# Kernel optimization log

Hardware: AMD Instinct MI355X
Metric: run time of the kernel (lower is better)

## Reference

```python
import jax, jax.numpy as jnp
import numpy as np
import math

NUM_HEADS = 16


def _alibi_slopes(n):
    # n is a power of 2 here (16)
    start = 2.0 ** (-2.0 ** (-(math.log2(n) - 3)))
    return jnp.asarray([start * (start ** i) for i in range(n)], dtype=jnp.float32)


def setup_inputs() -> dict:
    key = jax.random.key(0)
    ks = jax.random.split(key, 7)
    B, S, D = 2, 2048, 1024
    s = 0.02
    return {
        "query": jax.random.normal(ks[0], (B, S, D), jnp.float32),
        "key": jax.random.normal(ks[1], (B, S, D), jnp.float32),
        "value": jax.random.normal(ks[2], (B, S, D), jnp.float32),
        "Wq": jax.random.normal(ks[3], (D, D), jnp.float32) * s,
        "Wk": jax.random.normal(ks[4], (D, D), jnp.float32) * s,
        "Wv": jax.random.normal(ks[5], (D, D), jnp.float32) * s,
        "Wo": jax.random.normal(ks[6], (D, D), jnp.float32) * s,
    }


def reference(query, key, value, Wq, Wk, Wv, Wo):
    B, S, D = query.shape
    H = NUM_HEADS
    hd = D // H
    scale = math.sqrt(hd)

    # projections (bias-free linears), split into heads: [B, S, H, hd]
    Q = (query @ Wq).reshape(B, S, H, hd)
    K = (key @ Wk).reshape(B, -1, H, hd)
    V = (value @ Wv).reshape(B, -1, H, hd)

    # attention scores [B, H, S, S]
    scores = jnp.einsum("bqhd,bkhd->bhqk", Q, K) / scale

    # ALiBi bias: -slope_h * |i - j|, broadcast over batch
    pos = jnp.arange(S, dtype=jnp.float32)
    rel = jnp.abs(pos[None, :] - pos[:, None])  # [S, S]
    slopes = _alibi_slopes(H)
    scores = scores - slopes[None, :, None, None] * rel[None, None, :, :]

    attn = jax.nn.softmax(scores, axis=-1)
    out = jnp.einsum("bhqk,bkhd->bqhd", attn, V).reshape(B, S, D)
    return out @ Wo
```

## Files before the change

kernel.cpp:

```cpp
#include <hip/hip_runtime.h>
#include <cstdint>
#include <cstddef>


typedef unsigned short u16;
typedef __attribute__((ext_vector_type(8))) _Float16 half8;
typedef __attribute__((ext_vector_type(8))) unsigned short u16x8;
typedef __attribute__((ext_vector_type(4))) float f32x4;

#define DEVI static __device__ __forceinline__
#define MFMA16(a, b, c) __builtin_amdgcn_mfma_f32_16x16x32_f16(a, b, c, 0, 0, 0)

DEVI u16 f2h_bits(float f) {
  _Float16 h = (_Float16)f;
  union { _Float16 h; u16 u; } v; v.h = h;
  return v.u;
}

DEVI void gl_lds16(const u16* g, u16* l) {
  __builtin_amdgcn_global_load_lds(
      (const __attribute__((address_space(1))) void*)g,
      (__attribute__((address_space(3))) void*)l, 16, 0, 0);
}

__global__ __launch_bounds__(256) void cast3_h(const float* __restrict__ in0,
                                               const float* __restrict__ in1,
                                               const float* __restrict__ in2,
                                               u16* __restrict__ o0,
                                               u16* __restrict__ o1,
                                               u16* __restrict__ o2, int n) {
  const float* in = blockIdx.z == 0 ? in0 : (blockIdx.z == 1 ? in1 : in2);
  u16* out = blockIdx.z == 0 ? o0 : (blockIdx.z == 1 ? o1 : o2);
  int i = (blockIdx.x * 256 + threadIdx.x) * 4;
  if (i + 3 < n) {
    const float4 v = *(const float4*)(in + i);
    ushort4 o;
    o.x = f2h_bits(v.x); o.y = f2h_bits(v.y); o.z = f2h_bits(v.z); o.w = f2h_bits(v.w);
    *(ushort4*)(out + i) = o;
  }
}

__global__ __launch_bounds__(256) void transpose4_h(
    const float* __restrict__ W0, const float* __restrict__ W1,
    const float* __restrict__ W2, const float* __restrict__ W3,
    u16* __restrict__ T0, u16* __restrict__ T1, u16* __restrict__ T2,
    u16* __restrict__ T3) {
  const float* W = blockIdx.z == 0 ? W0 : (blockIdx.z == 1 ? W1 : (blockIdx.z == 2 ? W2 : W3));
  u16* Wt = blockIdx.z == 0 ? T0 : (blockIdx.z == 1 ? T1 : (blockIdx.z == 2 ? T2 : T3));
  __shared__ float tile[32][33];
  const int bx = blockIdx.x * 32;
  const int by = blockIdx.y * 32;
  const int x = threadIdx.x & 31;
  const int y0 = threadIdx.x >> 5;
#pragma unroll
  for (int i = y0; i < 32; i += 8)
    tile[i][x] = W[(size_t)(by + i) * 1024 + bx + x];
  __syncthreads();
#pragma unroll
  for (int i = y0; i < 32; i += 8)
    Wt[(size_t)(bx + i) * 1024 + by + x] = f2h_bits(tile[x][i]);
}

__global__ __launch_bounds__(256) void vtrans(const u16* __restrict__ Vp,
                                              u16* __restrict__ Vt) {
  __shared__ u16 tile[64][72];
  const int t = threadIdx.x;
  const int s0 = blockIdx.x * 64;
  const int bh = blockIdx.y;
  const int b = bh >> 4, h = bh & 15;
#pragma unroll
  for (int it = 0; it < 2; ++it) {
    const int ci = it * 256 + t;
    const int srow = ci >> 3, cc = (ci & 7) << 3;
    const u16x8 v = *(const u16x8*)(Vp + (size_t)(b * 2048 + s0 + srow) * 1024 + h * 64 + cc);
    *(u16x8*)(&tile[srow][cc]) = v;
  }
  __syncthreads();
#pragma unroll
  for (int it = 0; it < 2; ++it) {
    const int ci = it * 256 + t;
    const int drow = ci >> 3, cc = (ci & 7) << 3;
    u16x8 o;
#pragma unroll
    for (int j = 0; j < 8; ++j) o[j] = tile[cc + j][drow];
    *(u16x8*)(Vt + ((size_t)bh * 64 + drow) * 2048 + s0 + cc) = o;
  }
}

DEVI void gemm_body(const u16* __restrict__ A, const u16* __restrict__ Bt,
                    void* __restrict__ Cout, int mode, int kLo, int kHi,
                    u16* As, u16* Bs) {
  constexpr int K = 1024, N = 1024;
  const int t = threadIdx.x;
  const int lane = t & 63;
  const int quad = lane >> 4;
  const int l16 = lane & 15;
  const int wid = t >> 6;
  const int mBase = blockIdx.y * 128;
  const int nBase = blockIdx.x * 128;
  const int wM = (wid >> 1) * 64;
  const int wN = (wid & 1) * 64;
  const int cswz = l16 & 7;

  f32x4 acc[4][4];
#pragma unroll
  for (int i = 0; i < 4; ++i)
#pragma unroll
    for (int j = 0; j < 4; ++j) acc[i][j] = (f32x4){0.f, 0.f, 0.f, 0.f};

  for (int kt = kLo; kt < kHi; ++kt) {
    const int kB = kt * 64;
    __syncthreads();
#pragma unroll
    for (int i = 0; i < 4; ++i) {
      const int ci = i * 256 + t;
      const int row = ci >> 3;
      const int col = (((ci & 7) ^ (row & 7)) << 3);
      gl_lds16(A + (size_t)(mBase + row) * K + kB + col, As + ci * 8);
      gl_lds16(Bt + (size_t)(nBase + row) * K + kB + col, Bs + ci * 8);
    }
    __syncthreads();

#pragma unroll
    for (int kk = 0; kk < 2; ++kk) {
      const int ck = (((kk * 4 + quad) ^ cswz) << 3);
      half8 a[4], b[4];
#pragma unroll
      for (int mi = 0; mi < 4; ++mi)
        a[mi] = *(const half8*)(As + (wM + mi * 16 + l16) * 64 + ck);
#pragma unroll
      for (int ni = 0; ni < 4; ++ni)
        b[ni] = *(const half8*)(Bs + (wN + ni * 16 + l16) * 64 + ck);
#pragma unroll
      for (int mi = 0; mi < 4; ++mi)
#pragma unroll
        for (int ni = 0; ni < 4; ++ni)
          acc[mi][ni] = MFMA16(a[mi], b[ni], acc[mi][ni]);
    }
  }

#pragma unroll
  for (int mi = 0; mi < 4; ++mi) {
#pragma unroll
    for (int ni = 0; ni < 4; ++ni) {
#pragma unroll
      for (int r = 0; r < 4; ++r) {
        const int m = mBase + wM + mi * 16 + quad * 4 + r;
        const int n = nBase + wN + ni * 16 + l16;
        const float v = acc[mi][ni][r];
        if (mode == 0) {
          ((float*)Cout)[(size_t)m * N + n] = v;
        } else {
          ((u16*)Cout)[(size_t)m * N + n] = f2h_bits(v);
        }
      }
    }
  }
}

__global__ __launch_bounds__(256) void proj_qkv(
    const u16* __restrict__ qb, const u16* __restrict__ kb, const u16* __restrict__ vb,
    const u16* __restrict__ Wqt, const u16* __restrict__ Wkt, const u16* __restrict__ Wvt,
    u16* __restrict__ Qp, u16* __restrict__ Kp, u16* __restrict__ Vp) {
  __shared__ u16 As[128 * 64];
  __shared__ u16 Bs[128 * 64];
  const int z = blockIdx.z;
  const u16* A = z == 0 ? qb : (z == 1 ? kb : vb);
  const u16* Bt = z == 0 ? Wqt : (z == 1 ? Wkt : Wvt);
  void* C = z == 0 ? (void*)Qp : (z == 1 ? (void*)Kp : (void*)Vp);
  gemm_body(A, Bt, C, 1, 0, 16, As, Bs);
}

__global__ __launch_bounds__(256) void gemm_out(const u16* __restrict__ Ao,
                                                const u16* __restrict__ Wot,
                                                float* __restrict__ p0,
                                                float* __restrict__ p1) {
  __shared__ u16 As[128 * 64];
  __shared__ u16 Bs[128 * 64];
  const int z = blockIdx.z;
  gemm_body(Ao, Wot, z ? (void*)p1 : (void*)p0, 0, z * 8, z * 8 + 8, As, Bs);
}

__global__ __launch_bounds__(256) void add2(const float* __restrict__ a,
                                            const float* __restrict__ b,
                                            float* __restrict__ o, int n) {
  int i = (blockIdx.x * 256 + threadIdx.x) * 4;
  if (i + 3 < n) {
    float4 x = *(const float4*)(a + i);
    const float4 y = *(const float4*)(b + i);
    x.x += y.x; x.y += y.y; x.z += y.z; x.w += y.w;
    *(float4*)(o + i) = x;
  }
}

__global__ __launch_bounds__(128, 2) void flash_alibi(
    const u16* __restrict__ Qg, const u16* __restrict__ Kg,
    const u16* __restrict__ Vtg, u16* __restrict__ Opart,
    float* __restrict__ lpart) {
  constexpr int S = 2048, Dm = 1024, HD = 64;
  __shared__ u16 Qs[64 * 64];
  __shared__ u16 Ks[2][64 * 64];
  __shared__ u16 Vs[2][64 * 64];
  __shared__ u16 Ps[64 * 64];
  const int t = threadIdx.x, lane = t & 63, wid = t >> 6;
  const int quad = lane >> 4, l16 = lane & 15;
  const int idx = blockIdx.x;
  const int s = 29 - (idx >> 6);
  const int bq = idx & 63;
  const int b = bq >> 5, qt = bq & 31;
  int h, seg, nseg;
  if      (s >= 26) { h = 15; seg = s - 26; nseg = 4; }
  else if (s >= 22) { h = 14; seg = s - 22; nseg = 4; }
  else if (s >= 18) { h = 13; seg = s - 18; nseg = 4; }
  else if (s >= 15) { h = 12; seg = s - 15; nseg = 3; }
  else if (s >= 13) { h = 11; seg = s - 13; nseg = 2; }
  else if (s >= 11) { h = 10; seg = s - 11; nseg = 2; }
  else if (s >= 9)  { h = 9;  seg = s - 9;  nseg = 2; }
  else              { h = s;  seg = 0;      nseg = 1; }
  const int qBase = qt * 64;
  const size_t qRow0 = (size_t)b * S + qBase;
  const float sl2 = __builtin_amdgcn_exp2f(-0.5f * (float)(h + 1)) * 1.44269504f;
  const float sc2 = 0.125f * 1.44269504f;
  const int Di = (int)(22.0f / sl2);
  const int ktLo = max(0, (qBase - Di) >> 6);
  const int ktHi = min(31, (qBase + 63 + Di) >> 6);
  const int W = ktHi - ktLo + 1;
  const int myLo = ktLo + (W * seg) / nseg;
  const int myHi = ktLo + (W * (seg + 1)) / nseg - 1;
  const size_t slotG = (size_t)bq * 30 + s;
  const int cswz = ((l16 & 7) << 3);
  const u16* Kgb = Kg + (size_t)b * S * Dm + h * HD;
  const u16* Vgb = Vtg + (size_t)(b * 16 + h) * HD * S;

#pragma unroll
  for (int i = 0; i < 4; ++i) {
    const int ci = i * 128 + t;
    const int row = ci >> 3, col = (((ci & 7) ^ (row & 7)) << 3);
    gl_lds16(Qg + (qRow0 + row) * Dm + h * HD + col, Qs + ci * 8);
  }
  if (myLo <= myHi) {
#pragma unroll
    for (int i = 0; i < 4; ++i) {
      const int ci = i * 128 + t;
      const int row = ci >> 3, col = (((ci & 7) ^ (row & 7)) << 3);
      gl_lds16(Kgb + (size_t)(myLo * 64 + row) * Dm + col, Ks[0] + ci * 8);
      gl_lds16(Vgb + (size_t)row * S + myLo * 64 + col, Vs[0] + ci * 8);
    }
  }

  float bi[2][4];
#pragma unroll
  for (int m = 0; m < 2; ++m)
#pragma unroll
    for (int r = 0; r < 4; ++r)
      bi[m][r] = sl2 * (float)(qBase + wid * 32 + m * 16 + quad * 4 + r);

  f32x4 acc_o[2][4];
#pragma unroll
  for (int m = 0; m < 2; ++m)
#pragma unroll
    for (int nd = 0; nd < 4; ++nd) acc_o[m][nd] = (f32x4){0.f, 0.f, 0.f, 0.f};
  float lrow[2][4] = {{0.f, 0.f, 0.f, 0.f}, {0.f, 0.f, 0.f, 0.f}};

  const int pRowBase = wid * 32;
  int cur = 0;

  for (int kt = myLo; kt <= myHi; ++kt, cur ^= 1) {
    __asm__ volatile("s_waitcnt vmcnt(0) lgkmcnt(0)\n\ts_barrier" ::: "memory");

    if (kt < myHi) {
      const int kB2 = (kt + 1) * 64;
      u16* Kd = Ks[cur ^ 1];
      u16* Vd = Vs[cur ^ 1];
#pragma unroll
      for (int i = 0; i < 4; ++i) {
        const int ci = i * 128 + t;
        const int row = ci >> 3, col = (((ci & 7) ^ (row & 7)) << 3);
        gl_lds16(Kgb + (size_t)(kB2 + row) * Dm + col, Kd + ci * 8);
        gl_lds16(Vgb + (size_t)row * S + kB2 + col, Vd + ci * 8);
      }
    }

    const int kB = kt * 64;
    f32x4 sc[2][4];
#pragma unroll
    for (int m = 0; m < 2; ++m)
#pragma unroll
      for (int ni = 0; ni < 4; ++ni) sc[m][ni] = (f32x4){0.f, 0.f, 0.f, 0.f};
#pragma unroll
    for (int ks = 0; ks < 2; ++ks) {
      const int ck = ((ks * 4 + quad) << 3) ^ cswz;
      const half8 a0 = *(const half8*)(Qs + (wid * 32 + l16) * HD + ck);
      const half8 a1 = *(const half8*)(Qs + (wid * 32 + 16 + l16) * HD + ck);
#pragma unroll
      for (int ni = 0; ni < 4; ++ni) {
        const half8 bk = *(const half8*)(Ks[cur] + (ni * 16 + l16) * HD + ck);
        sc[0][ni] = MFMA16(a0, bk, sc[0][ni]);
        sc[1][ni] = MFMA16(a1, bk, sc[1][ni]);
      }
    }

    float bj[4];
#pragma unroll
    for (int ni = 0; ni < 4; ++ni) bj[ni] = sl2 * (float)(kB + ni * 16 + l16);
#pragma unroll
    for (int m = 0; m < 2; ++m) {
#pragma unroll
      for (int r = 0; r < 4; ++r) {
        float rs = 0.f;
        const int prow = (pRowBase + m * 16 + quad * 4 + r) * 64;
#pragma unroll
        for (int ni = 0; ni < 4; ++ni) {
          const float d = fabsf(bi[m][r] - bj[ni]);
          const float p = __builtin_amdgcn_exp2f(sc[m][ni][r] * sc2 - d);
          rs += p;
          Ps[prow + ((ni * 16 + l16) ^ (quad << 4))] = f2h_bits(p);
        }
        lrow[m][r] += rs;
      }
    }
    __asm__ volatile("s_waitcnt lgkmcnt(0)" ::: "memory");

#pragma unroll
    for (int ks = 0; ks < 2; ++ks) {
      const int pk = (ks * 32 + quad * 8) ^ ((l16 & 12) << 2);
      const int ck = ((ks * 4 + quad) << 3) ^ cswz;
      const half8 aP0 = *(const half8*)(Ps + (pRowBase + l16) * 64 + pk);
      const half8 aP1 = *(const half8*)(Ps + (pRowBase + 16 + l16) * 64 + pk);
#pragma unroll
      for (int nd = 0; nd < 4; ++nd) {
        const half8 bv = *(const half8*)(Vs[cur] + (nd * 16 + l16) * HD + ck);
        acc_o[0][nd] = MFMA16(aP0, bv, acc_o[0][nd]);
        acc_o[1][nd] = MFMA16(aP1, bv, acc_o[1][nd]);
      }
    }
  }

#pragma unroll
  for (int m = 0; m < 2; ++m) {
#pragma unroll
    for (int r = 0; r < 4; ++r) {
      float l = lrow[m][r];
      l += __shfl_xor(l, 1);
      l += __shfl_xor(l, 2);
      l += __shfl_xor(l, 4);
      l += __shfl_xor(l, 8);
      const int rloc = wid * 32 + m * 16 + quad * 4 + r;
      if (l16 == 0) lpart[slotG * 64 + rloc] = l;
#pragma unroll
      for (int nd = 0; nd < 4; ++nd)
        Opart[slotG * 4096 + rloc * 64 + nd * 16 + l16] = f2h_bits(acc_o[m][nd][r]);
    }
  }
}

__global__ __launch_bounds__(256) void flash_merge(
    const u16* __restrict__ Opart, const float* __restrict__ lpart,
    u16* __restrict__ Ao) {
  const int idx = blockIdx.x;
  const int h = idx & 15, bq = idx >> 4;
  const int b = bq >> 5, qt = bq & 31;
  int base, nseg;
  if      (h == 15) { base = 26; nseg = 4; }
  else if (h == 14) { base = 22; nseg = 4; }
  else if (h == 13) { base = 18; nseg = 4; }
  else if (h == 12) { base = 15; nseg = 3; }
  else if (h == 11) { base = 13; nseg = 2; }
  else if (h == 10) { base = 11; nseg = 2; }
  else if (h == 9)  { base = 9;  nseg = 2; }
  else              { base = h;  nseg = 1; }
  const int t = threadIdx.x;
  const int q = t >> 2, dB = (t & 3) * 16;
  float acc[16];
#pragma unroll
  for (int j = 0; j < 16; ++j) acc[j] = 0.f;
  float l = 0.f;
  for (int sg = 0; sg < nseg; ++sg) {
    const size_t slotG = (size_t)bq * 30 + base + sg;
    l += lpart[slotG * 64 + q];
    const u16* p = Opart + slotG * 4096 + q * 64 + dB;
    const half8 v0 = *(const half8*)p;
    const half8 v1 = *(const half8*)(p + 8);
#pragma unroll
    for (int j = 0; j < 8; ++j) {
      acc[j] += (float)v0[j];
      acc[8 + j] += (float)v1[j];
    }
  }
  const float inv = 1.f / l;
  u16x8 o0, o1;
#pragma unroll
  for (int j = 0; j < 8; ++j) {
    o0[j] = f2h_bits(acc[j] * inv);
    o1[j] = f2h_bits(acc[8 + j] * inv);
  }
  u16* dst = Ao + ((size_t)(b * 2048 + qt * 64 + q)) * 1024 + h * 64 + dB;
  *(u16x8*)dst = o0;
  *(u16x8*)(dst + 8) = o1;
}

extern "C" void kernel_launch(void* const* d_in, const int* in_sizes, int n_in,
                              void* d_out, int out_size, void* d_ws, size_t ws_size,
                              hipStream_t stream) {
  const float* q  = (const float*)d_in[0];
  const float* k  = (const float*)d_in[1];
  const float* v  = (const float*)d_in[2];
  const float* Wq = (const float*)d_in[3];
  const float* Wk = (const float*)d_in[4];
  const float* Wv = (const float*)d_in[5];
  const float* Wo = (const float*)d_in[6];
  char* ws = (char*)d_ws;
  const size_t MB = 1ull << 20;
  u16* qb  = (u16*)(ws + 0 * MB);
  u16* kb  = (u16*)(ws + 8 * MB);
  u16* vb  = (u16*)(ws + 16 * MB);
  u16* Wqt = (u16*)(ws + 24 * MB);
  u16* Wkt = (u16*)(ws + 26 * MB);
  u16* Wvt = (u16*)(ws + 28 * MB);
  u16* Wot = (u16*)(ws + 30 * MB);
  u16* Qp  = (u16*)(ws + 32 * MB);
  u16* Kp  = (u16*)(ws + 40 * MB);
  u16* Vp  = (u16*)(ws + 48 * MB);
  u16* Ao  = (u16*)(ws + 56 * MB);
  u16* Vt  = vb;
  u16*   Opart = (u16*)(ws + 0 * MB);
  float* lpart = (float*)(ws + 48 * MB);
  float* p0 = (float*)(ws + 0 * MB);
  float* p1 = (float*)(ws + 32 * MB);

  const int n = 2 * 2048 * 1024;
  cast3_h<<<dim3(n / 1024, 1, 3), 256, 0, stream>>>(q, k, v, qb, kb, vb, n);
  transpose4_h<<<dim3(32, 32, 4), 256, 0, stream>>>(Wq, Wk, Wv, Wo, Wqt, Wkt, Wvt, Wot);
  proj_qkv<<<dim3(8, 32, 3), 256, 0, stream>>>(qb, kb, vb, Wqt, Wkt, Wvt, Qp, Kp, Vp);
  vtrans<<<dim3(32, 32), 256, 0, stream>>>(Vp, Vt);
  flash_alibi<<<1920, 128, 0, stream>>>(Qp, Kp, Vt, Opart, lpart);
  flash_merge<<<1024, 256, 0, stream>>>(Opart, lpart, Ao);
  gemm_out<<<dim3(8, 32, 2), 256, 0, stream>>>(Ao, Wot, p0, p1);
  add2<<<4096, 256, 0, stream>>>(p0, p1, (float*)d_out, n);
}
```

Baseline: 245.9 us.

## Use 128-row query tiles with 4 waves and write single-segment heads directly

The flash attention block now covers 128 query rows with 256 threads, so each loaded K/V tile is reused by twice as many rows. The segment split across heads is rebalanced to 36 segments per query tile. Heads that need only one segment normalize and write straight to the attention output, so the merge kernel only runs for heads 7-15. The K/V double buffering is dropped in favour of a single buffer loaded between two barriers, which exposes load latency in exchange for less LDS use and higher occupancy.

```diff
diff --git a/kernel.cpp b/kernel.cpp
--- a/kernel.cpp
+++ b/kernel.cpp
@@ -193,60 +193,52 @@
   }
 }
 
-__global__ __launch_bounds__(128, 2) void flash_alibi(
+__global__ __launch_bounds__(256, 3) void flash_alibi(
     const u16* __restrict__ Qg, const u16* __restrict__ Kg,
-    const u16* __restrict__ Vtg, u16* __restrict__ Opart,
-    float* __restrict__ lpart) {
+    const u16* __restrict__ Vtg, u16* __restrict__ Ao,
+    u16* __restrict__ Opart, float* __restrict__ lpart) {
   constexpr int S = 2048, Dm = 1024, HD = 64;
-  __shared__ u16 Qs[64 * 64];
-  __shared__ u16 Ks[2][64 * 64];
-  __shared__ u16 Vs[2][64 * 64];
-  __shared__ u16 Ps[64 * 64];
+  __shared__ u16 Qs[128 * 64];
+  __shared__ u16 Ks[64 * 64];
+  __shared__ u16 Vs[64 * 64];
+  __shared__ u16 Ps[128 * 64];
   const int t = threadIdx.x, lane = t & 63, wid = t >> 6;
   const int quad = lane >> 4, l16 = lane & 15;
   const int idx = blockIdx.x;
-  const int s = 29 - (idx >> 6);
-  const int bq = idx & 63;
-  const int b = bq >> 5, qt = bq & 31;
+  const int s = 35 - (idx >> 5);
+  const int bq = idx & 31;
+  const int b = bq >> 4, qt = bq & 15;
   int h, seg, nseg;
-  if      (s >= 26) { h = 15; seg = s - 26; nseg = 4; }
-  else if (s >= 22) { h = 14; seg = s - 22; nseg = 4; }
-  else if (s >= 18) { h = 13; seg = s - 18; nseg = 4; }
-  else if (s >= 15) { h = 12; seg = s - 15; nseg = 3; }
-  else if (s >= 13) { h = 11; seg = s - 13; nseg = 2; }
-  else if (s >= 11) { h = 10; seg = s - 11; nseg = 2; }
-  else if (s >= 9)  { h = 9;  seg = s - 9;  nseg = 2; }
+  if      (s >= 32) { h = 15; seg = s - 32; nseg = 4; }
+  else if (s >= 28) { h = 14; seg = s - 28; nseg = 4; }
+  else if (s >= 24) { h = 13; seg = s - 24; nseg = 4; }
+  else if (s >= 20) { h = 12; seg = s - 20; nseg = 4; }
+  else if (s >= 16) { h = 11; seg = s - 16; nseg = 4; }
+  else if (s >= 13) { h = 10; seg = s - 13; nseg = 3; }
+  else if (s >= 11) { h = 9;  seg = s - 11; nseg = 2; }
+  else if (s >= 9)  { h = 8;  seg = s - 9;  nseg = 2; }
+  else if (s >= 7)  { h = 7;  seg = s - 7;  nseg = 2; }
   else              { h = s;  seg = 0;      nseg = 1; }
-  const int qBase = qt * 64;
+  const int qBase = qt * 128;
   const size_t qRow0 = (size_t)b * S + qBase;
   const float sl2 = __builtin_amdgcn_exp2f(-0.5f * (float)(h + 1)) * 1.44269504f;
   const float sc2 = 0.125f * 1.44269504f;
   const int Di = (int)(22.0f / sl2);
   const int ktLo = max(0, (qBase - Di) >> 6);
-  const int ktHi = min(31, (qBase + 63 + Di) >> 6);
+  const int ktHi = min(31, (qBase + 127 + Di) >> 6);
   const int W = ktHi - ktLo + 1;
   const int myLo = ktLo + (W * seg) / nseg;
   const int myHi = ktLo + (W * (seg + 1)) / nseg - 1;
-  const size_t slotG = (size_t)bq * 30 + s;
   const int cswz = ((l16 & 7) << 3);
   const u16* Kgb = Kg + (size_t)b * S * Dm + h * HD;
   const u16* Vgb = Vtg + (size_t)(b * 16 + h) * HD * S;
 
 #pragma unroll
   for (int i = 0; i < 4; ++i) {
-    const int ci = i * 128 + t;
+    const int ci = i * 256 + t;
     const int row = ci >> 3, col = (((ci & 7) ^ (row & 7)) << 3);
     gl_lds16(Qg + (qRow0 + row) * Dm + h * HD + col, Qs + ci * 8);
   }
-  if (myLo <= myHi) {
-#pragma unroll
-    for (int i = 0; i < 4; ++i) {
-      const int ci = i * 128 + t;
-      const int row = ci >> 3, col = (((ci & 7) ^ (row & 7)) << 3);
-      gl_lds16(Kgb + (size_t)(myLo * 64 + row) * Dm + col, Ks[0] + ci * 8);
-      gl_lds16(Vgb + (size_t)row * S + myLo * 64 + col, Vs[0] + ci * 8);
-    }
-  }
 
   float bi[2][4];
 #pragma unroll
@@ -263,23 +255,17 @@
   float lrow[2][4] = {{0.f, 0.f, 0.f, 0.f}, {0.f, 0.f, 0.f, 0.f}};
 
   const int pRowBase = wid * 32;
-  int cur = 0;
-
-  for (int kt = myLo; kt <= myHi; ++kt, cur ^= 1) {
-    __asm__ volatile("s_waitcnt vmcnt(0) lgkmcnt(0)\n\ts_barrier" ::: "memory");
-
-    if (kt < myHi) {
-      const int kB2 = (kt + 1) * 64;
-      u16* Kd = Ks[cur ^ 1];
-      u16* Vd = Vs[cur ^ 1];
-#pragma unroll
-      for (int i = 0; i < 4; ++i) {
-        const int ci = i * 128 + t;
-        const int row = ci >> 3, col = (((ci & 7) ^ (row & 7)) << 3);
-        gl_lds16(Kgb + (size_t)(kB2 + row) * Dm + col, Kd + ci * 8);
-        gl_lds16(Vgb + (size_t)row * S + kB2 + col, Vd + ci * 8);
-      }
-    }
+
+  for (int kt = myLo; kt <= myHi; ++kt) {
+    __syncthreads();
+#pragma unroll
+    for (int i = 0; i < 2; ++i) {
+      const int ci = i * 256 + t;
+      const int row = ci >> 3, col = (((ci & 7) ^ (row & 7)) << 3);
+      gl_lds16(Kgb + (size_t)(kt * 64 + row) * Dm + col, Ks + ci * 8);
+      gl_lds16(Vgb + (size_t)row * S + kt * 64 + col, Vs + ci * 8);
+    }
+    __syncthreads();
 
     const int kB = kt * 64;
     f32x4 sc[2][4];
@@ -294,7 +280,7 @@
       const half8 a1 = *(const half8*)(Qs + (wid * 32 + 16 + l16) * HD + ck);
 #pragma unroll
       for (int ni = 0; ni < 4; ++ni) {
-        const half8 bk = *(const half8*)(Ks[cur] + (ni * 16 + l16) * HD + ck);
+        const half8 bk = *(const half8*)(Ks + (ni * 16 + l16) * HD + ck);
         sc[0][ni] = MFMA16(a0, bk, sc[0][ni]);
         sc[1][ni] = MFMA16(a1, bk, sc[1][ni]);
       }
@@ -329,13 +315,14 @@
       const half8 aP1 = *(const half8*)(Ps + (pRowBase + 16 + l16) * 64 + pk);
 #pragma unroll
       for (int nd = 0; nd < 4; ++nd) {
-        const half8 bv = *(const half8*)(Vs[cur] + (nd * 16 + l16) * HD + ck);
+        const half8 bv = *(const half8*)(Vs + (nd * 16 + l16) * HD + ck);
         acc_o[0][nd] = MFMA16(aP0, bv, acc_o[0][nd]);
         acc_o[1][nd] = MFMA16(aP1, bv, acc_o[1][nd]);
       }
     }
   }
 
+  const size_t slotG = (size_t)bq * 29 + (s - 7);
 #pragma unroll
   for (int m = 0; m < 2; ++m) {
 #pragma unroll
@@ -346,10 +333,18 @@
       l += __shfl_xor(l, 4);
       l += __shfl_xor(l, 8);
       const int rloc = wid * 32 + m * 16 + quad * 4 + r;
-      if (l16 == 0) lpart[slotG * 64 + rloc] = l;
-#pragma unroll
-      for (int nd = 0; nd < 4; ++nd)
-        Opart[slotG * 4096 + rloc * 64 + nd * 16 + l16] = f2h_bits(acc_o[m][nd][r]);
+      if (nseg == 1) {
+        const float inv = 1.f / l;
+#pragma unroll
+        for (int nd = 0; nd < 4; ++nd)
+          Ao[(qRow0 + rloc) * Dm + h * HD + nd * 16 + l16] =
+              f2h_bits(acc_o[m][nd][r] * inv);
+      } else {
+        if (l16 == 0) lpart[slotG * 128 + rloc] = l;
+#pragma unroll
+        for (int nd = 0; nd < 4; ++nd)
+          Opart[slotG * 8192 + rloc * 64 + nd * 16 + l16] = f2h_bits(acc_o[m][nd][r]);
+      }
     }
   }
 }
@@ -358,45 +353,45 @@
     const u16* __restrict__ Opart, const float* __restrict__ lpart,
     u16* __restrict__ Ao) {
   const int idx = blockIdx.x;
-  const int h = idx & 15, bq = idx >> 4;
-  const int b = bq >> 5, qt = bq & 31;
+  const int bq = idx / 9, hm = idx - bq * 9;
+  const int h = 7 + hm;
+  const int b = bq >> 4, qt = bq & 15;
   int base, nseg;
-  if      (h == 15) { base = 26; nseg = 4; }
-  else if (h == 14) { base = 22; nseg = 4; }
-  else if (h == 13) { base = 18; nseg = 4; }
-  else if (h == 12) { base = 15; nseg = 3; }
-  else if (h == 11) { base = 13; nseg = 2; }
-  else if (h == 10) { base = 11; nseg = 2; }
-  else if (h == 9)  { base = 9;  nseg = 2; }
-  else              { base = h;  nseg = 1; }
+  if      (h == 15) { base = 32; nseg = 4; }
+  else if (h == 14) { base = 28; nseg = 4; }
+  else if (h == 13) { base = 24; nseg = 4; }
+  else if (h == 12) { base = 20; nseg = 4; }
+  else if (h == 11) { base = 16; nseg = 4; }
+  else if (h == 10) { base = 13; nseg = 3; }
+  else if (h == 9)  { base = 11; nseg = 2; }
+  else if (h == 8)  { base = 9;  nseg = 2; }
+  else              { base = 7;  nseg = 2; }
   const int t = threadIdx.x;
-  const int q = t >> 2, dB = (t & 3) * 16;
-  float acc[16];
-#pragma unroll
-  for (int j = 0; j < 16; ++j) acc[j] = 0.f;
+  const int q = t >> 1, d0 = (t & 1) * 32;
+  float acc[32];
+#pragma unroll
+  for (int j = 0; j < 32; ++j) acc[j] = 0.f;
   float l = 0.f;
   for (int sg = 0; sg < nseg; ++sg) {
-    const size_t slotG = (size_t)bq * 30 + base + sg;
-    l += lpart[slotG * 64 + q];
-    const u16* p = Opart + slotG * 4096 + q * 64 + dB;
-    const half8 v0 = *(const half8*)p;
-    const half8 v1 = *(const half8*)(p + 8);
-#pragma unroll
-    for (int j = 0; j < 8; ++j) {
-      acc[j] += (float)v0[j];
-      acc[8 + j] += (float)v1[j];
+    const size_t slotG = (size_t)bq * 29 + (base - 7) + sg;
+    l += lpart[slotG * 128 + q];
+    const u16* p = Opart + slotG * 8192 + q * 64 + d0;
+#pragma unroll
+    for (int c = 0; c < 4; ++c) {
+      const half8 v = *(const half8*)(p + c * 8);
+#pragma unroll
+      for (int j = 0; j < 8; ++j) acc[c * 8 + j] += (float)v[j];
     }
   }
   const float inv = 1.f / l;
-  u16x8 o0, o1;
-#pragma unroll
-  for (int j = 0; j < 8; ++j) {
-    o0[j] = f2h_bits(acc[j] * inv);
-    o1[j] = f2h_bits(acc[8 + j] * inv);
-  }
-  u16* dst = Ao + ((size_t)(b * 2048 + qt * 64 + q)) * 1024 + h * 64 + dB;
-  *(u16x8*)dst = o0;
-  *(u16x8*)(dst + 8) = o1;
+  u16* dst = Ao + ((size_t)(b * 2048 + qt * 128 + q)) * 1024 + h * 64 + d0;
+#pragma unroll
+  for (int c = 0; c < 4; ++c) {
+    u16x8 o;
+#pragma unroll
+    for (int j = 0; j < 8; ++j) o[j] = f2h_bits(acc[c * 8 + j] * inv);
+    *(u16x8*)(dst + c * 8) = o;
+  }
 }
 
 extern "C" void kernel_launch(void* const* d_in, const int* in_sizes, int n_in,
@@ -433,8 +428,8 @@
   transpose4_h<<<dim3(32, 32, 4), 256, 0, stream>>>(Wq, Wk, Wv, Wo, Wqt, Wkt, Wvt, Wot);
   proj_qkv<<<dim3(8, 32, 3), 256, 0, stream>>>(qb, kb, vb, Wqt, Wkt, Wvt, Qp, Kp, Vp);
   vtrans<<<dim3(32, 32), 256, 0, stream>>>(Vp, Vt);
-  flash_alibi<<<1920, 128, 0, stream>>>(Qp, Kp, Vt, Opart, lpart);
-  flash_merge<<<1024, 256, 0, stream>>>(Opart, lpart, Ao);
+  flash_alibi<<<1152, 256, 0, stream>>>(Qp, Kp, Vt, Ao, Opart, lpart);
+  flash_merge<<<288, 256, 0, stream>>>(Opart, lpart, Ao);
   gemm_out<<<dim3(8, 32, 2), 256, 0, stream>>>(Ao, Wot, p0, p1);
   add2<<<4096, 256, 0, stream>>>(p0, p1, (float*)d_out, n);
 }
```

Result: faster. 236.4 us (-3.9%).
